# Kernel optimization log

Hardware: AMD Instinct MI355X
Metric: run time of the kernel (lower is better)

The kernel has to match this reference:

```python
import jax, jax.numpy as jnp
import numpy as np

EMBED_DIM = 1024
NUM_HEADS = 16
HEAD_DIM = EMBED_DIM // NUM_HEADS
WINDOW = 128  # window_size: attend to [i-W, i+W]


def setup_inputs() -> dict:
    key = jax.random.key(0)
    ks = jax.random.split(key, 9)
    B, S, E = 4, 4096, EMBED_DIM
    s = 1.0 / np.sqrt(E)
    return {
        "x": jax.random.normal(ks[0], (B, S, E), jnp.float32),
        "Wq": jax.random.normal(ks[1], (E, E), jnp.float32) * s,
        "bq": jnp.zeros((E,), jnp.float32),
        "Wk": jax.random.normal(ks[2], (E, E), jnp.float32) * s,
        "bk": jnp.zeros((E,), jnp.float32),
        "Wv": jax.random.normal(ks[3], (E, E), jnp.float32) * s,
        "bv": jnp.zeros((E,), jnp.float32),
        "Wo": jax.random.normal(ks[4], (E, E), jnp.float32) * s,
        "bo": jnp.zeros((E,), jnp.float32),
    }


def reference(x, Wq, bq, Wk, bk, Wv, bv, Wo, bo):
    B, S, E = x.shape
    H, D, W = NUM_HEADS, HEAD_DIM, WINDOW
    scale = jnp.sqrt(jnp.asarray(D, x.dtype))

    def heads(t):  # [B,S,E] -> [B,H,S,D]
        return t.reshape(B, S, H, D).transpose(0, 2, 1, 3)

    q = heads(x @ Wq + bq)
    k = heads(x @ Wk + bk)
    v = heads(x @ Wv + bv)

    # window indices per query position: j = i + [-W..W], masked to [0, S)
    offs = jnp.arange(-W, W + 1)                 # [2W+1]
    idx = jnp.arange(S)[:, None] + offs[None, :]  # [S, 2W+1]
    valid = (idx >= 0) & (idx < S)
    idxc = jnp.clip(idx, 0, S - 1)

    k_win = k[:, :, idxc, :]  # [B,H,S,2W+1,D]
    v_win = v[:, :, idxc, :]

    scores = jnp.einsum('bhsd,bhswd->bhsw', q, k_win) / scale
    scores = jnp.where(valid[None, None], scores, jnp.asarray(-jnp.inf, scores.dtype))
    attn = jax.nn.softmax(scores, axis=-1)
    out = jnp.einsum('bhsw,bhswd->bhsd', attn, v_win)  # [B,H,S,D]

    out = out.transpose(0, 2, 1, 3).reshape(B, S, E)
    return out @ Wo + bo
```

## Files before the change

### kernel.cpp

```cpp
#include <hip/hip_runtime.h>
#include <hip/hip_bf16.h>
#include <type_traits>

typedef unsigned short u16;
typedef __attribute__((ext_vector_type(8))) short  s16x8;
typedef __attribute__((ext_vector_type(4))) short  s16x4;
typedef __attribute__((ext_vector_type(8))) __bf16 b16x8;
typedef __attribute__((ext_vector_type(4))) float  f32x4;

#define S_LEN 4096
#define NB    4
#define EMB   1024
#define NH    16
#define HD    64
#define NROWS (NB * S_LEN)
#define KDIM  1024

static __device__ __forceinline__ u16 f2b(float f) {
  __hip_bfloat16 h = __float2bfloat16(f);
  return __builtin_bit_cast(u16, h);
}

template <typename T, typename = void>
struct mfma_takes : std::false_type {};
template <typename T>
struct mfma_takes<T, std::void_t<decltype(__builtin_amdgcn_mfma_f32_16x16x32_bf16(
    std::declval<T>(), std::declval<T>(), std::declval<f32x4>(), 0, 0, 0))>> : std::true_type {};

template <typename AB>
static __device__ __forceinline__ f32x4 mfma_any(AB a, AB b, f32x4 c) {
  return __builtin_amdgcn_mfma_f32_16x16x32_bf16(a, b, c, 0, 0, 0);
}

template <typename S8 = s16x8, typename B8 = b16x8>
static __device__ __forceinline__ f32x4 MFMA_BF16(s16x8 a, s16x8 b, f32x4 c) {
  if constexpr (mfma_takes<S8>::value)
    return mfma_any<S8>(__builtin_bit_cast(S8, a), __builtin_bit_cast(S8, b), c);
  else
    return mfma_any<B8>(__builtin_bit_cast(B8, a), __builtin_bit_cast(B8, b), c);
}

static __device__ __forceinline__ void gld_lds16(const void* g, void* l) {
  __builtin_amdgcn_global_load_lds((const __attribute__((address_space(1))) void*)g,
                                   (__attribute__((address_space(3))) void*)l, 16, 0, 0);
}

__global__ __launch_bounds__(256) void cvt_x_kernel(const float* __restrict__ in,
                                                    u16* __restrict__ out) {
  long i = ((long)blockIdx.x * 256 + threadIdx.x) * 8;
  float4 a = *(const float4*)(in + i);
  float4 b = *(const float4*)(in + i + 4);
  s16x8 o;
  o[0] = (short)f2b(a.x); o[1] = (short)f2b(a.y); o[2] = (short)f2b(a.z); o[3] = (short)f2b(a.w);
  o[4] = (short)f2b(b.x); o[5] = (short)f2b(b.y); o[6] = (short)f2b(b.z); o[7] = (short)f2b(b.w);
  *(s16x8*)(out + i) = o;
}

__global__ __launch_bounds__(256) void transpose_cvt4_kernel(
    const float* __restrict__ W0, const float* __restrict__ W1,
    const float* __restrict__ W2, const float* __restrict__ W3,
    u16* __restrict__ D0, u16* __restrict__ D1, u16* __restrict__ D2, u16* __restrict__ D3) {
  __shared__ float tile[32][33];
  const float* W; u16* D;
  switch (blockIdx.z) {
    case 0:  W = W0; D = D0; break;
    case 1:  W = W1; D = D1; break;
    case 2:  W = W2; D = D2; break;
    default: W = W3; D = D3; break;
  }
  int n0 = blockIdx.x * 32, k0 = blockIdx.y * 32;
  int tx = threadIdx.x & 31, ty = threadIdx.x >> 5;
#pragma unroll
  for (int i = ty; i < 32; i += 8)
    tile[i][tx] = W[(long)(k0 + i) * EMB + n0 + tx];
  __syncthreads();
#pragma unroll
  for (int i = ty; i < 32; i += 8)
    D[(long)(n0 + i) * EMB + k0 + tx] = f2b(tile[tx][i]);
}

#define SA_(p,k) (((p)*2+(k))*8192)
#define SB_(p,k) (32768 + ((p)*2+(k))*8192)

__global__ __launch_bounds__(512, 2) void gemm8p_kernel(
    const u16* __restrict__ A, const u16* __restrict__ Bt,
    const float* __restrict__ b0, const float* __restrict__ b1, const float* __restrict__ b2,
    void* __restrict__ Cp, int N, int out_f32) {
  __shared__ __align__(16) u16 smem[65536];
  const int tid = threadIdx.x;
  const int w = tid >> 6, lane = tid & 63;
  const int wm = w >> 2, wn = w & 3;
  const int frow = lane & 15, fg = lane >> 4;

  const int nwg = gridDim.x;
  const int bid = ((int)blockIdx.x & 7) * (nwg >> 3) + ((int)blockIdx.x >> 3);
  const int nbn = N >> 8;
  const int bm = bid / nbn, bn = bid % nbn;

  int offA[8];
#pragma unroll
  for (int j = 0; j < 8; j++) {
    int row = wm * 128 + j * 16 + frow;
    offA[j] = row * 32 + ((fg ^ ((row ^ (row >> 2)) & 3)) << 3);
  }
  int offB[4];
#pragma unroll
  for (int j = 0; j < 4; j++) {
    int row = wn * 64 + j * 16 + frow;
    offB[j] = row * 32 + ((fg ^ ((row ^ (row >> 2)) & 3)) << 3);
  }
  int srow[2], soff[2];
#pragma unroll
  for (int L = 0; L < 2; L++) {
    int lin = L * 512 + tid;
    int r = lin >> 2;
    srow[L] = r;
    soff[L] = (((lin & 3) ^ ((r ^ (r >> 2)) & 3)) << 3);
  }
  const u16* Abase = A + (long)bm * 256 * KDIM;
  const u16* Bbase = Bt + (long)bn * 256 * KDIM;

  f32x4 acc[8][4];
#pragma unroll
  for (int m = 0; m < 8; m++)
#pragma unroll
    for (int n = 0; n < 4; n++) acc[m][n] = (f32x4)0.0f;

  auto STAGE = [&](const u16* gb, int kcol, int slot) {
#pragma unroll
    for (int L = 0; L < 2; L++)
      gld_lds16(gb + (long)srow[L] * KDIM + kcol + soff[L],
                &smem[slot + (L * 512 + w * 64) * 8]);
  };

  s16x8 af[4], bf[4];

  STAGE(Abase, 0,  SA_(0,0)); STAGE(Bbase, 0,  SB_(0,0));
  STAGE(Abase, 32, SA_(0,1)); STAGE(Bbase, 32, SB_(0,1));
  STAGE(Abase, 64, SA_(1,0)); STAGE(Bbase, 64, SB_(1,0));
  asm volatile("s_waitcnt vmcnt(8)" ::: "memory");
  asm volatile("s_barrier" ::: "memory");

#define PHASE(p, k, mh, RDB, GB, KCOL, SLOT, DOVM)                            \
  {                                                                           \
    if (RDB) {                                                                \
      _Pragma("unroll") for (int n = 0; n < 4; n++)                           \
        bf[n] = *(const s16x8*)&smem[SB_(p, k) + offB[n]];                    \
    }                                                                         \
    _Pragma("unroll") for (int m = 0; m < 4; m++)                             \
      af[m] = *(const s16x8*)&smem[SA_(p, k) + offA[(mh) * 4 + m]];           \
    STAGE(GB, KCOL, SLOT);                                                    \
    asm volatile("s_barrier" ::: "memory");                                   \
    asm volatile("s_waitcnt lgkmcnt(0)" ::: "memory");                        \
    __builtin_amdgcn_sched_barrier(0);                                        \
    __builtin_amdgcn_s_setprio(1);                                            \
    _Pragma("unroll") for (int m = 0; m < 4; m++)                             \
      _Pragma("unroll") for (int n = 0; n < 4; n++)                           \
        acc[(mh) * 4 + m][n] = MFMA_BF16(af[m], bf[n], acc[(mh) * 4 + m][n]); \
    __builtin_amdgcn_s_setprio(0);                                            \
    if (DOVM) asm volatile("s_waitcnt vmcnt(8)" ::: "memory");                \
    asm volatile("s_barrier" ::: "memory");                                   \
  }

#pragma unroll 1
  for (int i = 0; i < 8; i++) {
    const int t = 2 * i;
    const int k1 = ((t + 1) & 15) * 64;
    const int k2 = ((t + 2) & 15) * 64;
    const int k3 = ((t + 3) & 15) * 64;
    PHASE(0, 0, 0, 1, Abase, k1 + 32, SA_(1, 1), 0)
    PHASE(0, 0, 1, 0, Bbase, k1 + 32, SB_(1, 1), 1)
    PHASE(0, 1, 0, 1, Abase, k2,      SA_(0, 0), 0)
    PHASE(0, 1, 1, 0, Bbase, k2,      SB_(0, 0), 1)
    PHASE(1, 0, 0, 1, Abase, k2 + 32, SA_(0, 1), 0)
    PHASE(1, 0, 1, 0, Bbase, k2 + 32, SB_(0, 1), 1)
    PHASE(1, 1, 0, 1, Abase, k3,      SA_(1, 0), 0)
    PHASE(1, 1, 1, 0, Bbase, k3,      SB_(1, 0), 1)
  }
#undef PHASE

  asm volatile("s_waitcnt vmcnt(0)" ::: "memory");
  asm volatile("s_barrier" ::: "memory");

  const long crow0 = (long)(bm * 256) * N + bn * 256;
  if (!out_f32) {
    u16* buf = &smem[w * 4096];
#pragma unroll
    for (int mf = 0; mf < 8; mf++) {
#pragma unroll
      for (int n = 0; n < 4; n++) {
        int gc = bn * 256 + wn * 64 + n * 16 + frow;
        int which = gc >> 10;
        const float* bias = (which == 0) ? b0 : ((which == 1) ? b1 : b2);
        float bv = bias[gc & 1023];
#pragma unroll
        for (int r = 0; r < 4; r++)
          buf[(4 * fg + r) * 72 + n * 16 + frow] = f2b(acc[mf][n][r] + bv);
      }
      asm volatile("s_waitcnt lgkmcnt(0)" ::: "memory");
      __builtin_amdgcn_sched_barrier(0);
#pragma unroll
      for (int q = 0; q < 2; q++) {
        int row = q * 8 + (lane >> 3);
        int ch = lane & 7;
        s16x8 v = *(const s16x8*)&buf[row * 72 + ch * 8];
        long gr = (long)(wm * 128 + mf * 16 + row);
        *(s16x8*)((u16*)Cp + crow0 + gr * N + wn * 64 + ch * 8) = v;
      }
      asm volatile("s_waitcnt lgkmcnt(0)" ::: "memory");
      __builtin_amdgcn_sched_barrier(0);
    }
  } else {
    float* fbuf = (float*)&smem[w * 4096];
#pragma unroll
    for (int mf = 0; mf < 8; mf++) {
#pragma unroll
      for (int n = 0; n < 4; n++) {
        float bv = b0[(bn * 256 + wn * 64 + n * 16 + frow) & 1023];
#pragma unroll
        for (int r = 0; r < 4; r++)
          fbuf[(4 * fg + r) * 68 + n * 16 + frow] = acc[mf][n][r] + bv;
      }
      asm volatile("s_waitcnt lgkmcnt(0)" ::: "memory");
      __builtin_amdgcn_sched_barrier(0);
#pragma unroll
      for (int q = 0; q < 4; q++) {
        int row = q * 4 + (lane >> 4);
        int ch = lane & 15;
        float4 v = *(const float4*)&fbuf[row * 68 + ch * 4];
        long gr = (long)(wm * 128 + mf * 16 + row);
        *(float4*)((float*)Cp + crow0 + gr * N + wn * 64 + ch * 4) = v;
      }
      asm volatile("s_waitcnt lgkmcnt(0)" ::: "memory");
      __builtin_amdgcn_sched_barrier(0);
    }
  }
}

#define QBLK 128
#define LPITCH 72

__global__ __launch_bounds__(256) void attn_kernel(const u16* __restrict__ QKV,
                                                   u16* __restrict__ Oa) {
  __shared__ __align__(16) u16 smem[9216];
  u16* lK = smem;
  u16* lV = smem + 64 * LPITCH;

  const int tid = threadIdx.x;
  const int w = tid >> 6, lane = tid & 63;
  const int frow = lane & 15, fg = lane >> 4;

  const int nq = S_LEN / QBLK;
  int bid = (int)blockIdx.x;
  bid = (bid & 7) * ((NB * NH * nq) >> 3) + (bid >> 3);
  const int b = bid / (NH * nq);
  const int rem = bid % (NH * nq);
  const int h = rem / nq;
  const int qt = rem % nq;
  const int q0 = qt * QBLK;
  const int qw0 = q0 + 32 * w;

  const u16* base = QKV + (long)b * S_LEN * 3072 + h * 64;

  s16x8 qf[2][2];
#pragma unroll
  for (int m = 0; m < 2; m++)
#pragma unroll
    for (int kk = 0; kk < 2; kk++)
      qf[m][kk] = *(const s16x8*)(base + (long)(qw0 + 16 * m + frow) * 3072 + kk * 32 + 8 * fg);

  f32x4 acc[2][4];
#pragma unroll
  for (int m = 0; m < 2; m++)
#pragma unroll
    for (int n = 0; n < 4; n++) acc[m][n] = (f32x4)0.0f;
  float mrow[2] = {-1e30f, -1e30f};
  float lrow[2] = {0.f, 0.f};

  for (int t = 0; t < 6; t++) {
    const int kvb = q0 - 128 + t * 64;
    if (kvb + 63 < 0 || kvb >= S_LEN) continue;
    {
      const int srowt = tid >> 3;
      const int sc8 = tid & 7;
#pragma unroll
      for (int pass = 0; pass < 2; pass++) {
        int row = srowt + pass * 32;
        int kv = kvb + row;
        s16x8 kd = (s16x8)0, vd = (s16x8)0;
        if (kv >= 0 && kv < S_LEN) {
          kd = *(const s16x8*)(base + 1024 + (long)kv * 3072 + sc8 * 8);
          vd = *(const s16x8*)(base + 2048 + (long)kv * 3072 + sc8 * 8);
        }
        *(s16x8*)&lK[row * LPITCH + sc8 * 8] = kd;
        const int swz = row ^ (sc8 << 3);
#pragma unroll
        for (int j = 0; j < 8; j++) lV[(sc8 * 8 + j) * LPITCH + swz] = (u16)vd[j];
      }
    }
    __syncthreads();
    const bool active = (kvb + 63 >= qw0 - 128) && (kvb <= qw0 + 159);
    if (active) {
      f32x4 sfr[2][4];
#pragma unroll
      for (int m = 0; m < 2; m++)
#pragma unroll
        for (int n = 0; n < 4; n++) sfr[m][n] = (f32x4)0.0f;
#pragma unroll
      for (int kk = 0; kk < 2; kk++) {
        s16x8 kb[4];
#pragma unroll
        for (int n = 0; n < 4; n++)
          kb[n] = *(const s16x8*)&lK[(16 * n + frow) * LPITCH + (fg + 4 * kk) * 8];
#pragma unroll
        for (int m = 0; m < 2; m++)
#pragma unroll
          for (int n = 0; n < 4; n++)
            sfr[m][n] = MFMA_BF16(kb[n], qf[m][kk], sfr[m][n]);
      }
#pragma unroll
      for (int m = 0; m < 2; m++) {
        const int q = qw0 + 16 * m + frow;
        float p[4][4];
        float tmax = -1e30f;
#pragma unroll
        for (int n = 0; n < 4; n++)
#pragma unroll
          for (int r = 0; r < 4; r++) {
            int kv = kvb + 16 * n + 4 * fg + r;
            bool valid = (kv >= q - 128) && (kv <= q + 128) && (kv >= 0) && (kv < S_LEN);
            float xv = valid ? sfr[m][n][r] * 0.125f : -1e30f;
            p[n][r] = xv;
            tmax = fmaxf(tmax, xv);
          }
        tmax = fmaxf(tmax, __shfl_xor(tmax, 16));
        tmax = fmaxf(tmax, __shfl_xor(tmax, 32));
        float mold = mrow[m];
        float mnew = fmaxf(mold, tmax);
        float al = __expf(mold - mnew);
        mrow[m] = mnew;
        float ps = 0.f;
#pragma unroll
        for (int n = 0; n < 4; n++)
#pragma unroll
          for (int r = 0; r < 4; r++) {
            float e = (p[n][r] > -1e29f) ? __expf(p[n][r] - mnew) : 0.f;
            p[n][r] = e;
            ps += e;
          }
        ps += __shfl_xor(ps, 16);
        ps += __shfl_xor(ps, 32);
        lrow[m] = lrow[m] * al + ps;
        float a4[4];
#pragma unroll
        for (int r = 0; r < 4; r++) a4[r] = __shfl(al, 20 * fg + r);
#pragma unroll
        for (int nd = 0; nd < 4; nd++)
#pragma unroll
          for (int r = 0; r < 4; r++) acc[m][nd][r] *= a4[r];
#pragma unroll
        for (int kt = 0; kt < 2; kt++) {
          s16x8 pa;
#pragma unroll
          for (int j = 0; j < 8; j++)
            pa[j] = (short)f2b(p[2 * kt + (j >> 2)][j & 3]);
#pragma unroll
          for (int nd = 0; nd < 4; nd++) {
            const int d = 16 * nd + frow;
            const int key = ((d >> 3) & 7) << 3;
            const u16* vrow = &lV[d * LPITCH];
            const int a0 = (32 * kt + 4 * fg) ^ key;
            const int a1 = (32 * kt + 16 + 4 * fg) ^ key;
            s16x4 lo = *(const s16x4*)&vrow[a0];
            s16x4 hi = *(const s16x4*)&vrow[a1];
            s16x8 vb;
            vb[0] = lo[0]; vb[1] = lo[1]; vb[2] = lo[2]; vb[3] = lo[3];
            vb[4] = hi[0]; vb[5] = hi[1]; vb[6] = hi[2]; vb[7] = hi[3];
            acc[m][nd] = MFMA_BF16(pa, vb, acc[m][nd]);
          }
        }
      }
    }
    __syncthreads();
  }

  float i4[2][4];
#pragma unroll
  for (int m = 0; m < 2; m++) {
    float inv = 1.0f / lrow[m];
#pragma unroll
    for (int r = 0; r < 4; r++) i4[m][r] = __shfl(inv, 20 * fg + r);
  }
  u16* bb = smem + w * 2304;
#pragma unroll
  for (int m = 0; m < 2; m++)
#pragma unroll
    for (int nd = 0; nd < 4; nd++)
#pragma unroll
      for (int r = 0; r < 4; r++)
        bb[(16 * m + 4 * fg + r) * LPITCH + 16 * nd + frow] = f2b(acc[m][nd][r] * i4[m][r]);
  asm volatile("s_waitcnt lgkmcnt(0)" ::: "memory");
  __builtin_amdgcn_sched_barrier(0);
  u16* Ob = Oa + ((long)(b * S_LEN + qw0)) * EMB + h * HD;
#pragma unroll
  for (int i = 0; i < 4; i++) {
    int flat = lane + 64 * i;
    int row = flat >> 3, ch = flat & 7;
    *(s16x8*)(Ob + (long)row * EMB + ch * 8) = *(const s16x8*)&bb[row * LPITCH + ch * 8];
  }
}

extern "C" void kernel_launch(void* const* d_in, const int* in_sizes, int n_in,
                              void* d_out, int out_size, void* d_ws, size_t ws_size,
                              hipStream_t stream) {
  const float* x  = (const float*)d_in[0];
  const float* Wq = (const float*)d_in[1];
  const float* bq = (const float*)d_in[2];
  const float* Wk = (const float*)d_in[3];
  const float* bk = (const float*)d_in[4];
  const float* Wv = (const float*)d_in[5];
  const float* bv = (const float*)d_in[6];
  const float* Wo = (const float*)d_in[7];
  const float* bo = (const float*)d_in[8];

  char* ws = (char*)d_ws;
  u16* xb   = (u16*)ws;  ws += (size_t)NROWS * EMB * 2;
  u16* Wt   = (u16*)ws;  ws += (size_t)3 * EMB * EMB * 2;
  u16* Wot  = (u16*)ws;  ws += (size_t)EMB * EMB * 2;
  u16* QKVb = (u16*)ws;  ws += (size_t)NROWS * 3 * EMB * 2;
  u16* Oab  = (u16*)ws;  ws += (size_t)NROWS * EMB * 2;

  cvt_x_kernel<<<(NROWS * EMB) / (256 * 8), 256, 0, stream>>>(x, xb);

  dim3 tg(EMB / 32, EMB / 32, 4);
  transpose_cvt4_kernel<<<tg, 256, 0, stream>>>(
      Wq, Wk, Wv, Wo, Wt, Wt + (size_t)EMB * EMB, Wt + (size_t)2 * EMB * EMB, Wot);

  gemm8p_kernel<<<(NROWS / 256) * (3 * EMB / 256), 512, 0, stream>>>(
      xb, Wt, bq, bk, bv, QKVb, 3 * EMB, 0);

  attn_kernel<<<NB * NH * (S_LEN / QBLK), 256, 0, stream>>>(QKVb, Oab);

  gemm8p_kernel<<<(NROWS / 256) * (EMB / 256), 512, 0, stream>>>(
      Oab, Wot, bo, bo, bo, d_out, EMB, 1);
}
```

Measured before the change: 260.1 us.

## Emit head-major K and transposed V from QKV GEMM, async double-buffer attention loads

The QKV GEMM epilogue now writes Q row-major, K head-contiguous per (batch, head), and V transposed per head. This lets the attention kernel stage K/V tiles with direct global-to-LDS async loads into a double buffer instead of per-thread loads plus scalar V transposes. The GEMM's vmcnt waits are also relaxed and moved, and the LDS epilogue buffers use XOR swizzles instead of padding. In exchange, the V transpose moves into the GEMM epilogue, where each lane reads 32 scalar LDS entries, and the GEMM and attention pipelines now depend on the changed wait counts being correct.

```diff
diff --git a/kernel.cpp b/kernel.cpp
--- a/kernel.cpp
+++ b/kernel.cpp
@@ -15,6 +15,7 @@
 #define HD    64
 #define NROWS (NB * S_LEN)
 #define KDIM  1024
+#define BHSTRIDE (S_LEN * HD)
 
 static __device__ __forceinline__ u16 f2b(float f) {
   __hip_bfloat16 h = __float2bfloat16(f);
@@ -85,7 +86,8 @@
 __global__ __launch_bounds__(512, 2) void gemm8p_kernel(
     const u16* __restrict__ A, const u16* __restrict__ Bt,
     const float* __restrict__ b0, const float* __restrict__ b1, const float* __restrict__ b2,
-    void* __restrict__ Cp, int N, int out_f32) {
+    void* __restrict__ Cp, u16* __restrict__ Qb, u16* __restrict__ Kp, u16* __restrict__ Vt,
+    int N, int out_f32) {
   __shared__ __align__(16) u16 smem[65536];
   const int tid = threadIdx.x;
   const int w = tid >> 6, lane = tid & 63;
@@ -138,7 +140,7 @@
   STAGE(Abase, 0,  SA_(0,0)); STAGE(Bbase, 0,  SB_(0,0));
   STAGE(Abase, 32, SA_(0,1)); STAGE(Bbase, 32, SB_(0,1));
   STAGE(Abase, 64, SA_(1,0)); STAGE(Bbase, 64, SB_(1,0));
-  asm volatile("s_waitcnt vmcnt(8)" ::: "memory");
+  asm volatile("s_waitcnt vmcnt(4)" ::: "memory");
   asm volatile("s_barrier" ::: "memory");
 
 #define PHASE(p, k, mh, RDB, GB, KCOL, SLOT, DOVM)                            \
@@ -158,7 +160,7 @@
       _Pragma("unroll") for (int n = 0; n < 4; n++)                           \
         acc[(mh) * 4 + m][n] = MFMA_BF16(af[m], bf[n], acc[(mh) * 4 + m][n]); \
     __builtin_amdgcn_s_setprio(0);                                            \
-    if (DOVM) asm volatile("s_waitcnt vmcnt(8)" ::: "memory");                \
+    if (DOVM) asm volatile("s_waitcnt vmcnt(4)" ::: "memory");                \
     asm volatile("s_barrier" ::: "memory");                                   \
   }
 
@@ -169,11 +171,11 @@
     const int k2 = ((t + 2) & 15) * 64;
     const int k3 = ((t + 3) & 15) * 64;
     PHASE(0, 0, 0, 1, Abase, k1 + 32, SA_(1, 1), 0)
-    PHASE(0, 0, 1, 0, Bbase, k1 + 32, SB_(1, 1), 1)
+    PHASE(0, 0, 1, 0, Bbase, k1 + 32, SB_(1, 1), 0)
     PHASE(0, 1, 0, 1, Abase, k2,      SA_(0, 0), 0)
     PHASE(0, 1, 1, 0, Bbase, k2,      SB_(0, 0), 1)
     PHASE(1, 0, 0, 1, Abase, k2 + 32, SA_(0, 1), 0)
-    PHASE(1, 0, 1, 0, Bbase, k2 + 32, SB_(0, 1), 1)
+    PHASE(1, 0, 1, 0, Bbase, k2 + 32, SB_(0, 1), 0)
     PHASE(1, 1, 0, 1, Abase, k3,      SA_(1, 0), 0)
     PHASE(1, 1, 1, 0, Bbase, k3,      SB_(1, 0), 1)
   }
@@ -182,54 +184,88 @@
   asm volatile("s_waitcnt vmcnt(0)" ::: "memory");
   asm volatile("s_barrier" ::: "memory");
 
-  const long crow0 = (long)(bm * 256) * N + bn * 256;
+  const int Mbase = bm * 256 + wm * 128;
+
   if (!out_f32) {
-    u16* buf = &smem[w * 4096];
-#pragma unroll
-    for (int mf = 0; mf < 8; mf++) {
-#pragma unroll
-      for (int n = 0; n < 4; n++) {
-        int gc = bn * 256 + wn * 64 + n * 16 + frow;
-        int which = gc >> 10;
-        const float* bias = (which == 0) ? b0 : ((which == 1) ? b1 : b2);
-        float bv = bias[gc & 1023];
-#pragma unroll
-        for (int r = 0; r < 4; r++)
-          buf[(4 * fg + r) * 72 + n * 16 + frow] = f2b(acc[mf][n][r] + bv);
+    const int g = bn * 256 + wn * 64;
+    const int part = g >> 10;
+    const int head = (g & 1023) >> 6;
+    const float* bias = (part == 0) ? b0 : ((part == 1) ? b1 : b2);
+    float bv[4];
+#pragma unroll
+    for (int n = 0; n < 4; n++) bv[n] = bias[(g & 1023) + n * 16 + frow];
+    u16* buf = &smem[w * 2048];
+#pragma unroll
+    for (int mf2 = 0; mf2 < 4; mf2++) {
+#pragma unroll
+      for (int half = 0; half < 2; half++) {
+        const int mf = mf2 * 2 + half;
+#pragma unroll
+        for (int n = 0; n < 4; n++)
+#pragma unroll
+          for (int r = 0; r < 4; r++) {
+            int row32 = half * 16 + 4 * fg + r;
+            int col = n * 16 + frow;
+            buf[row32 * 64 + (((col >> 3) ^ (row32 & 7)) << 3) + (col & 7)] =
+                f2b(acc[mf][n][r] + bv[n]);
+          }
       }
       asm volatile("s_waitcnt lgkmcnt(0)" ::: "memory");
       __builtin_amdgcn_sched_barrier(0);
-#pragma unroll
-      for (int q = 0; q < 2; q++) {
-        int row = q * 8 + (lane >> 3);
-        int ch = lane & 7;
-        s16x8 v = *(const s16x8*)&buf[row * 72 + ch * 8];
-        long gr = (long)(wm * 128 + mf * 16 + row);
-        *(s16x8*)((u16*)Cp + crow0 + gr * N + wn * 64 + ch * 8) = v;
+      const int s0 = Mbase + mf2 * 32;
+      if (part == 2) {
+        const int d = lane;
+        u16 tmp[32];
+#pragma unroll
+        for (int r32 = 0; r32 < 32; r32++)
+          tmp[r32] = buf[r32 * 64 + (((d >> 3) ^ (r32 & 7)) << 3) + (d & 7)];
+        u16* dst = Vt + ((long)((s0 >> 12) * 16 + head)) * BHSTRIDE + (long)d * S_LEN + (s0 & 4095);
+#pragma unroll
+        for (int q = 0; q < 4; q++) {
+          s16x8 pk;
+#pragma unroll
+          for (int j = 0; j < 8; j++) pk[j] = (short)tmp[q * 8 + j];
+          *(s16x8*)(dst + q * 8) = pk;
+        }
+      } else {
+#pragma unroll
+        for (int i = 0; i < 4; i++) {
+          int flat = lane + 64 * i;
+          int row32 = flat >> 3, ch = flat & 7;
+          s16x8 v = *(const s16x8*)&buf[row32 * 64 + ((ch ^ (row32 & 7)) << 3)];
+          int s = s0 + row32;
+          u16* dst = (part == 0)
+              ? (Qb + (long)s * 1024 + head * 64 + ch * 8)
+              : (Kp + ((long)(s >> 12) * 16 + head) * BHSTRIDE + (long)(s & 4095) * 64 + ch * 8);
+          *(s16x8*)dst = v;
+        }
       }
       asm volatile("s_waitcnt lgkmcnt(0)" ::: "memory");
       __builtin_amdgcn_sched_barrier(0);
     }
   } else {
-    float* fbuf = (float*)&smem[w * 4096];
+    float* fbuf = (float*)&smem[w * 2048];
+    const long crow0 = (long)Mbase * N + bn * 256 + wn * 64;
 #pragma unroll
     for (int mf = 0; mf < 8; mf++) {
 #pragma unroll
       for (int n = 0; n < 4; n++) {
-        float bv = b0[(bn * 256 + wn * 64 + n * 16 + frow) & 1023];
-#pragma unroll
-        for (int r = 0; r < 4; r++)
-          fbuf[(4 * fg + r) * 68 + n * 16 + frow] = acc[mf][n][r] + bv;
+        float bvv = b0[(bn * 256 + wn * 64 + n * 16 + frow) & 1023];
+#pragma unroll
+        for (int r = 0; r < 4; r++) {
+          int row = 4 * fg + r;
+          int o = 4 * n + (frow >> 2);
+          fbuf[row * 64 + ((o ^ (row & 7)) << 2) + (frow & 3)] = acc[mf][n][r] + bvv;
+        }
       }
       asm volatile("s_waitcnt lgkmcnt(0)" ::: "memory");
       __builtin_amdgcn_sched_barrier(0);
 #pragma unroll
-      for (int q = 0; q < 4; q++) {
-        int row = q * 4 + (lane >> 4);
-        int ch = lane & 15;
-        float4 v = *(const float4*)&fbuf[row * 68 + ch * 4];
-        long gr = (long)(wm * 128 + mf * 16 + row);
-        *(float4*)((float*)Cp + crow0 + gr * N + wn * 64 + ch * 4) = v;
+      for (int i = 0; i < 4; i++) {
+        int flat = lane + 64 * i;
+        int row = flat >> 4, oct = lane & 15;
+        float4 v = *(const float4*)&fbuf[row * 64 + ((oct ^ (row & 7)) << 2)];
+        *(float4*)((float*)Cp + crow0 + (long)(mf * 16 + row) * N + oct * 4) = v;
       }
       asm volatile("s_waitcnt lgkmcnt(0)" ::: "memory");
       __builtin_amdgcn_sched_barrier(0);
@@ -238,13 +274,12 @@
 }
 
 #define QBLK 128
-#define LPITCH 72
-
-__global__ __launch_bounds__(256) void attn_kernel(const u16* __restrict__ QKV,
+
+__global__ __launch_bounds__(256) void attn_kernel(const u16* __restrict__ Qb,
+                                                   const u16* __restrict__ Kp,
+                                                   const u16* __restrict__ Vt,
                                                    u16* __restrict__ Oa) {
-  __shared__ __align__(16) u16 smem[9216];
-  u16* lK = smem;
-  u16* lV = smem + 64 * LPITCH;
+  __shared__ __align__(16) u16 smem[16384];
 
   const int tid = threadIdx.x;
   const int w = tid >> 6, lane = tid & 63;
@@ -260,14 +295,16 @@
   const int q0 = qt * QBLK;
   const int qw0 = q0 + 32 * w;
 
-  const u16* base = QKV + (long)b * S_LEN * 3072 + h * 64;
+  const u16* Kpb = Kp + (long)(b * NH + h) * BHSTRIDE;
+  const u16* Vtb = Vt + (long)(b * NH + h) * BHSTRIDE;
 
   s16x8 qf[2][2];
 #pragma unroll
   for (int m = 0; m < 2; m++)
 #pragma unroll
     for (int kk = 0; kk < 2; kk++)
-      qf[m][kk] = *(const s16x8*)(base + (long)(qw0 + 16 * m + frow) * 3072 + kk * 32 + 8 * fg);
+      qf[m][kk] = *(const s16x8*)(Qb + (long)(b * S_LEN + qw0 + 16 * m + frow) * 1024 +
+                                  h * 64 + kk * 32 + 8 * fg);
 
   f32x4 acc[2][4];
 #pragma unroll
@@ -277,30 +314,39 @@
   float mrow[2] = {-1e30f, -1e30f};
   float lrow[2] = {0.f, 0.f};
 
-  for (int t = 0; t < 6; t++) {
-    const int kvb = q0 - 128 + t * 64;
-    if (kvb + 63 < 0 || kvb >= S_LEN) continue;
-    {
-      const int srowt = tid >> 3;
-      const int sc8 = tid & 7;
-#pragma unroll
-      for (int pass = 0; pass < 2; pass++) {
-        int row = srowt + pass * 32;
-        int kv = kvb + row;
-        s16x8 kd = (s16x8)0, vd = (s16x8)0;
-        if (kv >= 0 && kv < S_LEN) {
-          kd = *(const s16x8*)(base + 1024 + (long)kv * 3072 + sc8 * 8);
-          vd = *(const s16x8*)(base + 2048 + (long)kv * 3072 + sc8 * 8);
-        }
-        *(s16x8*)&lK[row * LPITCH + sc8 * 8] = kd;
-        const int swz = row ^ (sc8 << 3);
-#pragma unroll
-        for (int j = 0; j < 8; j++) lV[(sc8 * 8 + j) * LPITCH + swz] = (u16)vd[j];
-      }
+  const int r8 = lane >> 3;
+  const int cs = ((lane & 7) ^ r8) << 3;
+
+  auto STAGE = [&](int kvb, int bufi) {
+#pragma unroll
+    for (int pass = 0; pass < 2; pass++) {
+      int rbase = pass * 32 + w * 8;
+      gld_lds16(Kpb + (long)(kvb + rbase + r8) * 64 + cs, &smem[bufi * 4096 + rbase * 64]);
+      gld_lds16(Vtb + (long)(rbase + r8) * S_LEN + kvb + cs, &smem[8192 + bufi * 4096 + rbase * 64]);
     }
-    __syncthreads();
+  };
+
+  const int tlo = (q0 == 0) ? 2 : 0;
+  const int thi = (q0 == S_LEN - QBLK) ? 3 : 5;
+
+  STAGE(q0 - 128 + 64 * tlo, 0);
+
+#pragma unroll 1
+  for (int t = tlo; t <= thi; t++) {
+    const int cur = (t - tlo) & 1;
+    const int kvb = q0 - 128 + 64 * t;
+    if (t < thi) {
+      STAGE(kvb + 64, cur ^ 1);
+      asm volatile("s_waitcnt vmcnt(4)" ::: "memory");
+    } else {
+      asm volatile("s_waitcnt vmcnt(0)" ::: "memory");
+    }
+    asm volatile("s_barrier" ::: "memory");
+
     const bool active = (kvb + 63 >= qw0 - 128) && (kvb <= qw0 + 159);
     if (active) {
+      const u16* lK = &smem[cur * 4096];
+      const u16* lV = &smem[8192 + cur * 4096];
       f32x4 sfr[2][4];
 #pragma unroll
       for (int m = 0; m < 2; m++)
@@ -311,7 +357,7 @@
         s16x8 kb[4];
 #pragma unroll
         for (int n = 0; n < 4; n++)
-          kb[n] = *(const s16x8*)&lK[(16 * n + frow) * LPITCH + (fg + 4 * kk) * 8];
+          kb[n] = *(const s16x8*)&lK[(16 * n + frow) * 64 + (((fg + 4 * kk) ^ (frow & 7)) << 3)];
 #pragma unroll
         for (int m = 0; m < 2; m++)
 #pragma unroll
@@ -367,12 +413,11 @@
 #pragma unroll
           for (int nd = 0; nd < 4; nd++) {
             const int d = 16 * nd + frow;
-            const int key = ((d >> 3) & 7) << 3;
-            const u16* vrow = &lV[d * LPITCH];
-            const int a0 = (32 * kt + 4 * fg) ^ key;
-            const int a1 = (32 * kt + 16 + 4 * fg) ^ key;
-            s16x4 lo = *(const s16x4*)&vrow[a0];
-            s16x4 hi = *(const s16x4*)&vrow[a1];
+            const int key = frow & 7;
+            const int olo = (4 * kt + (fg >> 1)) ^ key;
+            const int ohi = (4 * kt + 2 + (fg >> 1)) ^ key;
+            s16x4 lo = *(const s16x4*)&lV[d * 64 + olo * 8 + (fg & 1) * 4];
+            s16x4 hi = *(const s16x4*)&lV[d * 64 + ohi * 8 + (fg & 1) * 4];
             s16x8 vb;
             vb[0] = lo[0]; vb[1] = lo[1]; vb[2] = lo[2]; vb[3] = lo[3];
             vb[4] = hi[0]; vb[5] = hi[1]; vb[6] = hi[2]; vb[7] = hi[3];
@@ -381,7 +426,7 @@
         }
       }
     }
-    __syncthreads();
+    asm volatile("s_barrier" ::: "memory");
   }
 
   float i4[2][4];
@@ -391,22 +436,27 @@
 #pragma unroll
     for (int r = 0; r < 4; r++) i4[m][r] = __shfl(inv, 20 * fg + r);
   }
-  u16* bb = smem + w * 2304;
+  u16* bb = &smem[w * 2048];
 #pragma unroll
   for (int m = 0; m < 2; m++)
 #pragma unroll
     for (int nd = 0; nd < 4; nd++)
 #pragma unroll
-      for (int r = 0; r < 4; r++)
-        bb[(16 * m + 4 * fg + r) * LPITCH + 16 * nd + frow] = f2b(acc[m][nd][r] * i4[m][r]);
+      for (int r = 0; r < 4; r++) {
+        int row32 = 16 * m + 4 * fg + r;
+        int col = 16 * nd + frow;
+        bb[row32 * 64 + (((col >> 3) ^ (row32 & 7)) << 3) + (col & 7)] =
+            f2b(acc[m][nd][r] * i4[m][r]);
+      }
   asm volatile("s_waitcnt lgkmcnt(0)" ::: "memory");
   __builtin_amdgcn_sched_barrier(0);
   u16* Ob = Oa + ((long)(b * S_LEN + qw0)) * EMB + h * HD;
 #pragma unroll
   for (int i = 0; i < 4; i++) {
     int flat = lane + 64 * i;
-    int row = flat >> 3, ch = flat & 7;
-    *(s16x8*)(Ob + (long)row * EMB + ch * 8) = *(const s16x8*)&bb[row * LPITCH + ch * 8];
+    int row32 = flat >> 3, ch = flat & 7;
+    s16x8 v = *(const s16x8*)&bb[row32 * 64 + ((ch ^ (row32 & 7)) << 3)];
+    *(s16x8*)(Ob + (long)row32 * EMB + ch * 8) = v;
   }
 }
 
@@ -427,7 +477,9 @@
   u16* xb   = (u16*)ws;  ws += (size_t)NROWS * EMB * 2;
   u16* Wt   = (u16*)ws;  ws += (size_t)3 * EMB * EMB * 2;
   u16* Wot  = (u16*)ws;  ws += (size_t)EMB * EMB * 2;
-  u16* QKVb = (u16*)ws;  ws += (size_t)NROWS * 3 * EMB * 2;
+  u16* Qbuf = (u16*)ws;  ws += (size_t)NROWS * EMB * 2;
+  u16* Kpb  = (u16*)ws;  ws += (size_t)NB * NH * BHSTRIDE * 2;
+  u16* Vtb  = (u16*)ws;  ws += (size_t)NB * NH * BHSTRIDE * 2;
   u16* Oab  = (u16*)ws;  ws += (size_t)NROWS * EMB * 2;
 
   cvt_x_kernel<<<(NROWS * EMB) / (256 * 8), 256, 0, stream>>>(x, xb);
@@ -437,10 +489,10 @@
       Wq, Wk, Wv, Wo, Wt, Wt + (size_t)EMB * EMB, Wt + (size_t)2 * EMB * EMB, Wot);
 
   gemm8p_kernel<<<(NROWS / 256) * (3 * EMB / 256), 512, 0, stream>>>(
-      xb, Wt, bq, bk, bv, QKVb, 3 * EMB, 0);
-
-  attn_kernel<<<NB * NH * (S_LEN / QBLK), 256, 0, stream>>>(QKVb, Oab);
+      xb, Wt, bq, bk, bv, nullptr, Qbuf, Kpb, Vtb, 3 * EMB, 0);
+
+  attn_kernel<<<NB * NH * (S_LEN / QBLK), 256, 0, stream>>>(Qbuf, Kpb, Vtb, Oab);
 
   gemm8p_kernel<<<(NROWS / 256) * (EMB / 256), 512, 0, stream>>>(
-      Oab, Wot, bo, bo, bo, d_out, EMB, 1);
-}
+      Oab, Wot, bo, bo, bo, d_out, nullptr, nullptr, nullptr, EMB, 1);
+}
```

Result: slower. 275.5 us (+5.9%).
